# Optimization experiments

Measured on AMD Instinct MI355X. Metric: run time of the kernel, lower is better.

The kernel has to match this reference:

```python
import jax, jax.numpy as jnp
import numpy as np

B, T, IN, HID, LAT = 256, 512, 128, 64, 16

def _mk_lstm(key, in_dim, h_dim, scale):
    k1, k2, k3, k4 = jax.random.split(key, 4)
    return (jax.random.normal(k1, (4 * h_dim, in_dim), jnp.float32) * scale,
            jax.random.normal(k2, (4 * h_dim, h_dim), jnp.float32) * scale,
            jax.random.normal(k3, (4 * h_dim,), jnp.float32) * scale,
            jax.random.normal(k4, (4 * h_dim,), jnp.float32) * scale)

def setup_inputs() -> dict:
    key = jax.random.key(0)
    ks = jax.random.split(key, 5)
    x = jax.random.normal(ks[0], (B, T, IN), jnp.float32)
    out = {"x": x}
    dims = [(IN, HID, "e1"), (HID, LAT, "e2"), (LAT, HID, "d1"), (HID, IN, "d2")]
    for k, (di, dh, nm) in zip(ks[1:], dims):
        scale = 1.0 / np.sqrt(dh)  # pytorch LSTM init range ~ 1/sqrt(hidden)
        Wih, Whh, bih, bhh = _mk_lstm(k, di, dh, scale)
        out[f"Wih_{nm}"], out[f"Whh_{nm}"], out[f"bih_{nm}"], out[f"bhh_{nm}"] = Wih, Whh, bih, bhh
    return out

def lstm(x, Wih, Whh, bih, bhh):
    # x: [B,T,I]; gates ordered i,f,g,o as in torch.nn.LSTM
    H = Whh.shape[1]
    xg = jnp.einsum('bti,gi->btg', x, Wih) + bih + bhh  # [B,T,4H]
    def step(carry, xt):
        h, c = carry
        g = xt + h @ Whh.T
        i, f, gg, o = jnp.split(g, 4, axis=-1)
        c = jax.nn.sigmoid(f) * c + jax.nn.sigmoid(i) * jnp.tanh(gg)
        h = jax.nn.sigmoid(o) * jnp.tanh(c)
        return (h, c), h
    b = x.shape[0]
    h0 = jnp.zeros((b, H), x.dtype)
    _, hs = jax.lax.scan(step, (h0, h0), jnp.swapaxes(xg, 0, 1))
    return jnp.swapaxes(hs, 0, 1)  # [B,T,H]

def reference(x, Wih_e1, Whh_e1, bih_e1, bhh_e1, Wih_e2, Whh_e2, bih_e2, bhh_e2,
              Wih_d1, Whh_d1, bih_d1, bhh_d1, Wih_d2, Whh_d2, bih_d2, bhh_d2):
    # dropout layers are identity at inference
    out = jax.nn.relu(lstm(x, Wih_e1, Whh_e1, bih_e1, bhh_e1))
    out = jax.nn.relu(lstm(out, Wih_e2, Whh_e2, bih_e2, bhh_e2))
    latent = out[:, -1, :]                                  # [B,LAT]
    dec_in = jnp.broadcast_to(latent[:, None, :], (x.shape[0], x.shape[1], latent.shape[-1]))
    out = jax.nn.relu(lstm(dec_in, Wih_d1, Whh_d1, bih_d1, bhh_d1))
    return lstm(out, Wih_d2, Whh_d2, bih_d2, bhh_d2)        # [B,T,IN]
```

## Files before the change

kernel.cpp:

```cpp
#include <hip/hip_runtime.h>


#define BB 256
#define TT 512

typedef _Float16 half2v __attribute__((ext_vector_type(2)));

static __device__ __forceinline__ float dot2(half2v a, half2v b, float c){
  return __builtin_amdgcn_fdot2(a,b,c,false);
}
template<int CTRL>
static __device__ __forceinline__ float qb(float v){
  return __int_as_float(__builtin_amdgcn_update_dpp(0, __float_as_int(v), CTRL, 0xF, 0xF, true));
}
static __device__ __forceinline__ float qsum1(float v){ return v + qb<0xB1>(v); }
static __device__ __forceinline__ float qsum2(float v){ return v + qb<0x4E>(v); }
static __device__ __forceinline__ float hsum8(float v){
  v = qsum1(v); v = qsum2(v); return v + qb<0x141>(v);
}
static __device__ __forceinline__ unsigned packh2(float lo, float hi){
  half2v p; p.x=(_Float16)lo; p.y=(_Float16)hi;
  return __builtin_bit_cast(unsigned, p);
}
static __device__ __forceinline__ half2v ash2(unsigned u){ return __builtin_bit_cast(half2v,u); }
static __device__ __forceinline__ half2v mkh2(float lo, float hi){
  half2v p; p.x=(_Float16)lo; p.y=(_Float16)hi; return p;
}

static __device__ __forceinline__ float lstm_update(int q, float a0, float a1,
                                                    float a2, float a3, float& c){
  float mine = a0;
  mine = (q==1) ? a1 : mine;
  mine = (q==2) ? a2 : mine;
  mine = (q==3) ? a3 : mine;
  const bool isg = (q==2);
  const float arg = isg ? (mine+mine) : mine;
  const float s   = 1.0f/(1.0f + __expf(-arg));
  const float act = isg ? (s+s-1.0f) : s;
  const float bi = qb<0x00>(act);
  const float bf = qb<0x55>(act);
  const float bg = qb<0xAA>(act);
  const float bo = qb<0xFF>(act);
  c = bf*c + bi*bg;
  const float s2 = 1.0f/(1.0f + __expf(-(c+c)));
  return bo*(s2+s2-1.0f);
}

__global__ void __launch_bounds__(512, 2) k_fused(
    const float* __restrict__ x,
    const float* __restrict__ WihE1, const float* __restrict__ WhhE1,
    const float* __restrict__ bihE1, const float* __restrict__ bhhE1,
    const float* __restrict__ WihE2, const float* __restrict__ WhhE2,
    const float* __restrict__ bihE2, const float* __restrict__ bhhE2,
    const float* __restrict__ WihD1, const float* __restrict__ WhhD1,
    const float* __restrict__ bihD1, const float* __restrict__ bhhD1,
    const float* __restrict__ WihD2, const float* __restrict__ WhhD2,
    const float* __restrict__ bihD2, const float* __restrict__ bhhD2,
    float* __restrict__ out)
{
  const int b = blockIdx.x, tid = threadIdx.x;

  __shared__ unsigned wD1L[8*1024];
  __shared__ unsigned vhE [2*96];
  __shared__ unsigned e2op[2*48];
  __shared__ unsigned dop [2*96];
  __shared__ unsigned vhD1[2*32];
  __shared__ float4   bD2L[128];
  __shared__ float4   pD1L[64];
  __shared__ float    latF[16];

  {
    const int o = tid & 7, j = tid >> 3;
    half2v w1[4][12];
    float bias1[4];
#pragma unroll
    for (int g=0; g<4; ++g){
      const int row = g*64 + j;
      bias1[g] = (o==0) ? (bihE1[row]+bhhE1[row]) : 0.0f;
#pragma unroll
      for (int m=0;m<12;++m){
        const int k0 = 24*o + 2*m;
        const float lo = (k0   < 128)? WihE1[row*128+k0]   : WhhE1[row*64 + (k0-128)];
        const float hi = (k0+1 < 128)? WihE1[row*128+k0+1] : WhhE1[row*64 + (k0+1-128)];
        w1[g][m] = mkh2(lo,hi);
      }
    }
    const bool e2act = (tid >= 64 && tid < 128);
    const int q2 = tid & 3, j2 = (tid - 64) >> 2;
    half2v w2[4][12];
    float bias2[4] = {0.f,0.f,0.f,0.f};
    if (e2act){
#pragma unroll
      for (int g=0; g<4; ++g){
        const int row = g*16 + j2;
        bias2[g] = (q2==0) ? (bihE2[row]+bhhE2[row]) : 0.0f;
#pragma unroll
        for (int m=0;m<12;++m){
          const int k0 = 24*q2 + 2*m;
          float lo = 0.0f, hi = 0.0f;
          if (k0 < 64)        lo = WihE2[row*64+k0];
          else if (k0 < 80)   lo = WhhE2[row*16 + (k0-64)];
          if (k0+1 < 64)      hi = WihE2[row*64+k0+1];
          else if (k0+1 < 80) hi = WhhE2[row*16 + (k0+1-64)];
          w2[g][m] = mkh2(lo,hi);
        }
      }
    }
    const bool xact = (tid < 64);
    const float* xrow = x + (size_t)b * (TT*128);
    float2 xa, xb;
    if (xact){
      float2 v0 = *(const float2*)(xrow + 2*tid);
      vhE[tid] = packh2(v0.x, v0.y);
      xa = *(const float2*)(xrow + 128 + 2*tid);
      xb = *(const float2*)(xrow + 256 + 2*tid);
    }
    if (tid >= 128 && tid < 160) vhE[64 + (tid-128)] = 0u;
    if (tid >= 160 && tid < 256) e2op[tid-160] = 0u;
    float c1 = 0.0f, c2 = 0.0f;
    __syncthreads();

#define XSTAGE(T, NXT) do{ if (xact){                                          \
      vhE[(NXT)*96 + tid] = packh2(xa.x, xa.y);                                \
      xa = xb;                                                                 \
      const int t3_ = ((T)+3 < TT) ? ((T)+3) : (TT-1);                         \
      xb = *(const float2*)(xrow + (size_t)t3_*128 + 2*tid);                   \
    } }while(0)

#define E1STEP(T, CUR) do{                                                     \
      float a0=bias1[0], a1=bias1[1], a2=bias1[2], a3=bias1[3];                \
      const uint4* vp = (const uint4*)(vhE + (CUR)*96 + o*12);                 \
      _Pragma("unroll")                                                        \
      for (int r=0;r<3;++r){                                                   \
        const uint4 u = vp[r];                                                 \
        const half2v o0=ash2(u.x), o1=ash2(u.y), o2=ash2(u.z), o3=ash2(u.w);   \
        a0=dot2(w1[0][4*r+0],o0,a0); a1=dot2(w1[1][4*r+0],o0,a1);              \
        a2=dot2(w1[2][4*r+0],o0,a2); a3=dot2(w1[3][4*r+0],o0,a3);              \
        a0=dot2(w1[0][4*r+1],o1,a0); a1=dot2(w1[1][4*r+1],o1,a1);              \
        a2=dot2(w1[2][4*r+1],o1,a2); a3=dot2(w1[3][4*r+1],o1,a3);              \
        a0=dot2(w1[0][4*r+2],o2,a0); a1=dot2(w1[1][4*r+2],o2,a1);              \
        a2=dot2(w1[2][4*r+2],o2,a2); a3=dot2(w1[3][4*r+2],o2,a3);              \
        a0=dot2(w1[0][4*r+3],o3,a0); a1=dot2(w1[1][4*r+3],o3,a1);              \
        a2=dot2(w1[2][4*r+3],o3,a2); a3=dot2(w1[3][4*r+3],o3,a3);              \
      }                                                                        \
      a0=hsum8(a0); a1=hsum8(a1); a2=hsum8(a2); a3=hsum8(a3);                  \
      const float h = lstm_update(o & 3, a0, a1, a2, a3, c1);                  \
      if (o == 0){                                                             \
        ((_Float16*)(vhE + ((CUR)^1)*96))[128 + j] = (_Float16)h;              \
        ((_Float16*)(e2op + (CUR)*48))[j]          = (_Float16)fmaxf(h, 0.0f); \
      }                                                                        \
    }while(0)

#define E2STEP(T2, CP) do{ if (e2act){                                         \
      float a0=bias2[0], a1=bias2[1], a2=bias2[2], a3=bias2[3];                \
      const uint4* vp = (const uint4*)(e2op + (CP)*48 + q2*12);                \
      _Pragma("unroll")                                                        \
      for (int r=0;r<3;++r){                                                   \
        const uint4 u = vp[r];                                                 \
        const half2v o0=ash2(u.x), o1=ash2(u.y), o2=ash2(u.z), o3=ash2(u.w);   \
        a0=dot2(w2[0][4*r+0],o0,a0); a1=dot2(w2[1][4*r+0],o0,a1);              \
        a2=dot2(w2[2][4*r+0],o0,a2); a3=dot2(w2[3][4*r+0],o0,a3);              \
        a0=dot2(w2[0][4*r+1],o1,a0); a1=dot2(w2[1][4*r+1],o1,a1);              \
        a2=dot2(w2[2][4*r+1],o1,a2); a3=dot2(w2[3][4*r+1],o1,a3);              \
        a0=dot2(w2[0][4*r+2],o2,a0); a1=dot2(w2[1][4*r+2],o2,a1);              \
        a2=dot2(w2[2][4*r+2],o2,a2); a3=dot2(w2[3][4*r+2],o2,a3);              \
        a0=dot2(w2[0][4*r+3],o3,a0); a1=dot2(w2[1][4*r+3],o3,a1);              \
        a2=dot2(w2[2][4*r+3],o3,a2); a3=dot2(w2[3][4*r+3],o3,a3);              \
      }                                                                        \
      a0=qsum2(qsum1(a0)); a1=qsum2(qsum1(a1));                                \
      a2=qsum2(qsum1(a2)); a3=qsum2(qsum1(a3));                                \
      const float h = lstm_update(q2, a0, a1, a2, a3, c2);                     \
      if (q2 == 0){                                                            \
        ((_Float16*)(e2op + ((CP)^1)*48))[64 + j2] = (_Float16)h;              \
        if ((T2) == TT-1) latF[j2] = fmaxf(h, 0.0f);                           \
      }                                                                        \
    } }while(0)

    XSTAGE(0, 1); E1STEP(0, 0);
    __syncthreads();
    for (int t = 1; t <= TT-3; t += 2){
      XSTAGE(t, 0);   E1STEP(t, 1);   E2STEP(t-1, 0);
      __syncthreads();
      XSTAGE(t+1, 1); E1STEP(t+1, 0); E2STEP(t, 1);
      __syncthreads();
    }
    XSTAGE(TT-1, 0); E1STEP(TT-1, 1); E2STEP(TT-2, 0);
    __syncthreads();
    E2STEP(TT-1, 1);
    __syncthreads();
#undef XSTAGE
#undef E1STEP
#undef E2STEP
  }
  __syncthreads();
  asm volatile("" ::: "memory");

  {
#pragma unroll
    for (int i=0;i<16;++i){
      const int idx = i*512 + tid;
      const int r = idx >> 10, rem = idx & 1023, l = rem >> 2, d = rem & 3;
      const int jd_ = l >> 2, qd_ = l & 3, g = r >> 1, m = ((r & 1) << 2) + d;
      const int row = g*64 + jd_, k0 = qd_*16 + 2*m;
      wD1L[idx] = packh2(WhhD1[row*64+k0], WhhD1[row*64+k0+1]);
    }
    if (tid < 128){
      float4 bb;
      bb.x = bihD2[0*128+tid] + bhhD2[0*128+tid];
      bb.y = bihD2[1*128+tid] + bhhD2[1*128+tid];
      bb.z = bihD2[2*128+tid] + bhhD2[2*128+tid];
      bb.w = bihD2[3*128+tid] + bhhD2[3*128+tid];
      bD2L[tid] = bb;
    }
    if (tid < 64){
      float4 pp;
#pragma unroll
      for (int g=0; g<4; ++g){
        const int row = g*64 + tid;
        float a = bihD1[row] + bhhD1[row];
#pragma unroll
        for (int i=0;i<16;++i) a = fmaf(WihD1[row*16+i], latF[i], a);
        (&pp.x)[g] = a;
      }
      pD1L[tid] = pp;
    }

    const int qd = tid & 3, jd = tid >> 2;
    half2v wD2[4][24];
#pragma unroll
    for (int g=0; g<4; ++g){
      const int row = g*128 + jd;
#pragma unroll
      for (int m=0;m<24;++m){
        const int k0 = 48*qd + 2*m;
        const float lo = (k0   < 64)? WihD2[row*64+k0]   : WhhD2[row*128+(k0-64)];
        const float hi = (k0+1 < 64)? WihD2[row*64+k0+1] : WhhD2[row*128+(k0+1-64)];
        wD2[g][m] = mkh2(lo,hi);
      }
    }
    const bool d1act = (tid < 256);
    if (tid < 64)                dop[32 + tid] = 0u;
    if (tid >= 64 && tid < 96)   vhD1[tid-64] = 0u;
    float cd1 = 0.0f, cd2 = 0.0f;
    float* orow = out + (size_t)b * (TT*128);
    __syncthreads();

#define D2STEP(T2, C2P) do{                                                    \
      float a0=0.f, a1=0.f, a2=0.f, a3=0.f;                                    \
      const uint4* vp = (const uint4*)(dop + (C2P)*96 + qd*24);                \
      _Pragma("unroll")                                                        \
      for (int r=0;r<6;++r){                                                   \
        const uint4 u = vp[r];                                                 \
        const half2v o0=ash2(u.x),o1=ash2(u.y),o2=ash2(u.z),o3=ash2(u.w);      \
        a0=dot2(wD2[0][4*r+0],o0,a0); a1=dot2(wD2[1][4*r+0],o0,a1);            \
        a2=dot2(wD2[2][4*r+0],o0,a2); a3=dot2(wD2[3][4*r+0],o0,a3);            \
        a0=dot2(wD2[0][4*r+1],o1,a0); a1=dot2(wD2[1][4*r+1],o1,a1);            \
        a2=dot2(wD2[2][4*r+1],o1,a2); a3=dot2(wD2[3][4*r+1],o1,a3);            \
        a0=dot2(wD2[0][4*r+2],o2,a0); a1=dot2(wD2[1][4*r+2],o2,a1);            \
        a2=dot2(wD2[2][4*r+2],o2,a2); a3=dot2(wD2[3][4*r+2],o2,a3);            \
        a0=dot2(wD2[0][4*r+3],o3,a0); a1=dot2(wD2[1][4*r+3],o3,a1);            \
        a2=dot2(wD2[2][4*r+3],o3,a2); a3=dot2(wD2[3][4*r+3],o3,a3);            \
      }                                                                        \
      a0=qsum2(qsum1(a0)); a1=qsum2(qsum1(a1));                                \
      a2=qsum2(qsum1(a2)); a3=qsum2(qsum1(a3));                                \
      const float4 bb = bD2L[jd];                                              \
      a0 += bb.x; a1 += bb.y; a2 += bb.z; a3 += bb.w;                          \
      const float h = lstm_update(qd, a0, a1, a2, a3, cd2);                    \
      if (qd==0){                                                              \
        ((_Float16*)(dop + ((C2P)^1)*96))[64 + jd] = (_Float16)h;              \
        orow[(size_t)(T2)*128 + jd] = h;                                       \
      }                                                                        \
    }while(0)

#define D1STEP(T, CUR) do{ if (d1act){                                         \
      const uint4* ov = (const uint4*)(vhD1 + (CUR)*32 + qd*8);                \
      const uint4 o01 = ov[0], o23 = ov[1];                                    \
      float a0=0.f, a1=0.f, a2=0.f, a3=0.f;                                    \
      {                                                                        \
        const uint4 wA = *(const uint4*)(wD1L + 0*1024 + tid*4);               \
        const uint4 wB = *(const uint4*)(wD1L + 1*1024 + tid*4);               \
        a0=dot2(ash2(wA.x),ash2(o01.x),a0); a0=dot2(ash2(wA.y),ash2(o01.y),a0);\
        a0=dot2(ash2(wA.z),ash2(o01.z),a0); a0=dot2(ash2(wA.w),ash2(o01.w),a0);\
        a0=dot2(ash2(wB.x),ash2(o23.x),a0); a0=dot2(ash2(wB.y),ash2(o23.y),a0);\
        a0=dot2(ash2(wB.z),ash2(o23.z),a0); a0=dot2(ash2(wB.w),ash2(o23.w),a0);\
      }                                                                        \
      {                                                                        \
        const uint4 wA = *(const uint4*)(wD1L + 2*1024 + tid*4);               \
        const uint4 wB = *(const uint4*)(wD1L + 3*1024 + tid*4);               \
        a1=dot2(ash2(wA.x),ash2(o01.x),a1); a1=dot2(ash2(wA.y),ash2(o01.y),a1);\
        a1=dot2(ash2(wA.z),ash2(o01.z),a1); a1=dot2(ash2(wA.w),ash2(o01.w),a1);\
        a1=dot2(ash2(wB.x),ash2(o23.x),a1); a1=dot2(ash2(wB.y),ash2(o23.y),a1);\
        a1=dot2(ash2(wB.z),ash2(o23.z),a1); a1=dot2(ash2(wB.w),ash2(o23.w),a1);\
      }                                                                        \
      {                                                                        \
        const uint4 wA = *(const uint4*)(wD1L + 4*1024 + tid*4);               \
        const uint4 wB = *(const uint4*)(wD1L + 5*1024 + tid*4);               \
        a2=dot2(ash2(wA.x),ash2(o01.x),a2); a2=dot2(ash2(wA.y),ash2(o01.y),a2);\
        a2=dot2(ash2(wA.z),ash2(o01.z),a2); a2=dot2(ash2(wA.w),ash2(o01.w),a2);\
        a2=dot2(ash2(wB.x),ash2(o23.x),a2); a2=dot2(ash2(wB.y),ash2(o23.y),a2);\
        a2=dot2(ash2(wB.z),ash2(o23.z),a2); a2=dot2(ash2(wB.w),ash2(o23.w),a2);\
      }                                                                        \
      {                                                                        \
        const uint4 wA = *(const uint4*)(wD1L + 6*1024 + tid*4);               \
        const uint4 wB = *(const uint4*)(wD1L + 7*1024 + tid*4);               \
        a3=dot2(ash2(wA.x),ash2(o01.x),a3); a3=dot2(ash2(wA.y),ash2(o01.y),a3);\
        a3=dot2(ash2(wA.z),ash2(o01.z),a3); a3=dot2(ash2(wA.w),ash2(o01.w),a3);\
        a3=dot2(ash2(wB.x),ash2(o23.x),a3); a3=dot2(ash2(wB.y),ash2(o23.y),a3);\
        a3=dot2(ash2(wB.z),ash2(o23.z),a3); a3=dot2(ash2(wB.w),ash2(o23.w),a3);\
      }                                                                        \
      a0=qsum2(qsum1(a0)); a1=qsum2(qsum1(a1));                                \
      a2=qsum2(qsum1(a2)); a3=qsum2(qsum1(a3));                                \
      const float4 pj = pD1L[jd];                                              \
      a0 += pj.x; a1 += pj.y; a2 += pj.z; a3 += pj.w;                          \
      const float h = lstm_update(qd, a0, a1, a2, a3, cd1);                    \
      if (qd==0){                                                              \
        ((_Float16*)(vhD1 + ((CUR)^1)*32))[jd] = (_Float16)h;                  \
        ((_Float16*)(dop + (CUR)*96))[jd]      = (_Float16)fmaxf(h,0.0f);      \
      }                                                                        \
    } }while(0)

    D1STEP(0, 0);
    __syncthreads();
    for (int t = 1; t <= TT-3; t += 2){
      D2STEP(t-1, 0); D1STEP(t, 1);
      __syncthreads();
      D2STEP(t, 1);   D1STEP(t+1, 0);
      __syncthreads();
    }
    D2STEP(TT-2, 0); D1STEP(TT-1, 1);
    __syncthreads();
    D2STEP(TT-1, 1);
#undef D2STEP
#undef D1STEP
  }
}

extern "C" void kernel_launch(void* const* d_in, const int* in_sizes, int n_in,
                              void* d_out, int out_size, void* d_ws, size_t ws_size,
                              hipStream_t stream) {
  const float* x      = (const float*)d_in[0];
  const float* WihE1  = (const float*)d_in[1];
  const float* WhhE1  = (const float*)d_in[2];
  const float* bihE1  = (const float*)d_in[3];
  const float* bhhE1  = (const float*)d_in[4];
  const float* WihE2  = (const float*)d_in[5];
  const float* WhhE2  = (const float*)d_in[6];
  const float* bihE2  = (const float*)d_in[7];
  const float* bhhE2  = (const float*)d_in[8];
  const float* WihD1  = (const float*)d_in[9];
  const float* WhhD1  = (const float*)d_in[10];
  const float* bihD1  = (const float*)d_in[11];
  const float* bhhD1  = (const float*)d_in[12];
  const float* WihD2  = (const float*)d_in[13];
  const float* WhhD2  = (const float*)d_in[14];
  const float* bihD2  = (const float*)d_in[15];
  const float* bhhD2  = (const float*)d_in[16];
  float* out = (float*)d_out;

  k_fused<<<BB, 512, 0, stream>>>(x,
      WihE1, WhhE1, bihE1, bhhE1,
      WihE2, WhhE2, bihE2, bhhE2,
      WihD1, WhhD1, bihD1, bhhD1,
      WihD2, WhhD2, bihD2, bhhD2,
      out);
}
```

Before: 871.9 us.

## Hold D1 recurrent weights in registers across all 512 threads and spread x staging

Decoder layer 1's recurrent weights now live in registers rather than a 32 KB shared-memory table. The work is spread over all 512 threads, each with 8 lanes per hidden unit and an 8-lane DPP reduction, replacing 256 threads that read weights from LDS on every step. The x-staging loads are also spread across one 8-lane group in each wave instead of the first 64 threads. The aim is to cut per-step LDS traffic and free shared memory, at the cost of extra VGPRs and an extra reduction stage on the critical recurrent path.

After: 984.8 us. 13.0% more time.

```diff
diff --git a/kernel.cpp b/kernel.cpp
--- a/kernel.cpp
+++ b/kernel.cpp
@@ -60,7 +60,6 @@
 {
   const int b = blockIdx.x, tid = threadIdx.x;
 
-  __shared__ unsigned wD1L[8*1024];
   __shared__ unsigned vhE [2*96];
   __shared__ unsigned e2op[2*48];
   __shared__ unsigned dop [2*96];
@@ -106,14 +105,15 @@
         }
       }
     }
-    const bool xact = (tid < 64);
+    const bool xact = ((tid & 63) < 8);
+    const int  xl   = ((tid >> 6) << 3) | (tid & 7);
     const float* xrow = x + (size_t)b * (TT*128);
     float2 xa, xb;
     if (xact){
-      float2 v0 = *(const float2*)(xrow + 2*tid);
-      vhE[tid] = packh2(v0.x, v0.y);
-      xa = *(const float2*)(xrow + 128 + 2*tid);
-      xb = *(const float2*)(xrow + 256 + 2*tid);
+      float2 v0 = *(const float2*)(xrow + 2*xl);
+      vhE[xl] = packh2(v0.x, v0.y);
+      xa = *(const float2*)(xrow + 128 + 2*xl);
+      xb = *(const float2*)(xrow + 256 + 2*xl);
     }
     if (tid >= 128 && tid < 160) vhE[64 + (tid-128)] = 0u;
     if (tid >= 160 && tid < 256) e2op[tid-160] = 0u;
@@ -121,10 +121,10 @@
     __syncthreads();
 
 #define XSTAGE(T, NXT) do{ if (xact){                                          \
-      vhE[(NXT)*96 + tid] = packh2(xa.x, xa.y);                                \
+      vhE[(NXT)*96 + xl] = packh2(xa.x, xa.y);                                 \
       xa = xb;                                                                 \
       const int t3_ = ((T)+3 < TT) ? ((T)+3) : (TT-1);                         \
-      xb = *(const float2*)(xrow + (size_t)t3_*128 + 2*tid);                   \
+      xb = *(const float2*)(xrow + (size_t)t3_*128 + 2*xl);                    \
     } }while(0)
 
 #define E1STEP(T, CUR) do{                                                     \
@@ -196,14 +196,6 @@
   asm volatile("" ::: "memory");
 
   {
-#pragma unroll
-    for (int i=0;i<16;++i){
-      const int idx = i*512 + tid;
-      const int r = idx >> 10, rem = idx & 1023, l = rem >> 2, d = rem & 3;
-      const int jd_ = l >> 2, qd_ = l & 3, g = r >> 1, m = ((r & 1) << 2) + d;
-      const int row = g*64 + jd_, k0 = qd_*16 + 2*m;
-      wD1L[idx] = packh2(WhhD1[row*64+k0], WhhD1[row*64+k0+1]);
-    }
     if (tid < 128){
       float4 bb;
       bb.x = bihD2[0*128+tid] + bhhD2[0*128+tid];
@@ -238,7 +230,17 @@
         wD2[g][m] = mkh2(lo,hi);
       }
     }
-    const bool d1act = (tid < 256);
+    const int o8 = tid & 7, j1d = tid >> 3;
+    half2v wd1[4][4];
+#pragma unroll
+    for (int g=0; g<4; ++g){
+      const int row = g*64 + j1d;
+#pragma unroll
+      for (int m=0;m<4;++m){
+        const int k0 = o8*8 + 2*m;
+        wd1[g][m] = mkh2(WhhD1[row*64+k0], WhhD1[row*64+k0+1]);
+      }
+    }
     if (tid < 64)                dop[32 + tid] = 0u;
     if (tid >= 64 && tid < 96)   vhD1[tid-64] = 0u;
     float cd1 = 0.0f, cd2 = 0.0f;
@@ -272,52 +274,27 @@
       }                                                                        \
     }while(0)
 
-#define D1STEP(T, CUR) do{ if (d1act){                                         \
-      const uint4* ov = (const uint4*)(vhD1 + (CUR)*32 + qd*8);                \
-      const uint4 o01 = ov[0], o23 = ov[1];                                    \
+#define D1STEP(T, CUR) do{                                                     \
+      const uint4 u = *(const uint4*)(vhD1 + (CUR)*32 + o8*4);                 \
+      const half2v o0=ash2(u.x),o1=ash2(u.y),o2=ash2(u.z),o3=ash2(u.w);        \
       float a0=0.f, a1=0.f, a2=0.f, a3=0.f;                                    \
-      {                                                                        \
-        const uint4 wA = *(const uint4*)(wD1L + 0*1024 + tid*4);               \
-        const uint4 wB = *(const uint4*)(wD1L + 1*1024 + tid*4);               \
-        a0=dot2(ash2(wA.x),ash2(o01.x),a0); a0=dot2(ash2(wA.y),ash2(o01.y),a0);\
-        a0=dot2(ash2(wA.z),ash2(o01.z),a0); a0=dot2(ash2(wA.w),ash2(o01.w),a0);\
-        a0=dot2(ash2(wB.x),ash2(o23.x),a0); a0=dot2(ash2(wB.y),ash2(o23.y),a0);\
-        a0=dot2(ash2(wB.z),ash2(o23.z),a0); a0=dot2(ash2(wB.w),ash2(o23.w),a0);\
-      }                                                                        \
-      {                                                                        \
-        const uint4 wA = *(const uint4*)(wD1L + 2*1024 + tid*4);               \
-        const uint4 wB = *(const uint4*)(wD1L + 3*1024 + tid*4);               \
-        a1=dot2(ash2(wA.x),ash2(o01.x),a1); a1=dot2(ash2(wA.y),ash2(o01.y),a1);\
-        a1=dot2(ash2(wA.z),ash2(o01.z),a1); a1=dot2(ash2(wA.w),ash2(o01.w),a1);\
-        a1=dot2(ash2(wB.x),ash2(o23.x),a1); a1=dot2(ash2(wB.y),ash2(o23.y),a1);\
-        a1=dot2(ash2(wB.z),ash2(o23.z),a1); a1=dot2(ash2(wB.w),ash2(o23.w),a1);\
-      }                                                                        \
-      {                                                                        \
-        const uint4 wA = *(const uint4*)(wD1L + 4*1024 + tid*4);               \
-        const uint4 wB = *(const uint4*)(wD1L + 5*1024 + tid*4);               \
-        a2=dot2(ash2(wA.x),ash2(o01.x),a2); a2=dot2(ash2(wA.y),ash2(o01.y),a2);\
-        a2=dot2(ash2(wA.z),ash2(o01.z),a2); a2=dot2(ash2(wA.w),ash2(o01.w),a2);\
-        a2=dot2(ash2(wB.x),ash2(o23.x),a2); a2=dot2(ash2(wB.y),ash2(o23.y),a2);\
-        a2=dot2(ash2(wB.z),ash2(o23.z),a2); a2=dot2(ash2(wB.w),ash2(o23.w),a2);\
-      }                                                                        \
-      {                                                                        \
-        const uint4 wA = *(const uint4*)(wD1L + 6*1024 + tid*4);               \
-        const uint4 wB = *(const uint4*)(wD1L + 7*1024 + tid*4);               \
-        a3=dot2(ash2(wA.x),ash2(o01.x),a3); a3=dot2(ash2(wA.y),ash2(o01.y),a3);\
-        a3=dot2(ash2(wA.z),ash2(o01.z),a3); a3=dot2(ash2(wA.w),ash2(o01.w),a3);\
-        a3=dot2(ash2(wB.x),ash2(o23.x),a3); a3=dot2(ash2(wB.y),ash2(o23.y),a3);\
-        a3=dot2(ash2(wB.z),ash2(o23.z),a3); a3=dot2(ash2(wB.w),ash2(o23.w),a3);\
-      }                                                                        \
-      a0=qsum2(qsum1(a0)); a1=qsum2(qsum1(a1));                                \
-      a2=qsum2(qsum1(a2)); a3=qsum2(qsum1(a3));                                \
-      const float4 pj = pD1L[jd];                                              \
+      a0=dot2(wd1[0][0],o0,a0); a1=dot2(wd1[1][0],o0,a1);                      \
+      a2=dot2(wd1[2][0],o0,a2); a3=dot2(wd1[3][0],o0,a3);                      \
+      a0=dot2(wd1[0][1],o1,a0); a1=dot2(wd1[1][1],o1,a1);                      \
+      a2=dot2(wd1[2][1],o1,a2); a3=dot2(wd1[3][1],o1,a3);                      \
+      a0=dot2(wd1[0][2],o2,a0); a1=dot2(wd1[1][2],o2,a1);                      \
+      a2=dot2(wd1[2][2],o2,a2); a3=dot2(wd1[3][2],o2,a3);                      \
+      a0=dot2(wd1[0][3],o3,a0); a1=dot2(wd1[1][3],o3,a1);                      \
+      a2=dot2(wd1[2][3],o3,a2); a3=dot2(wd1[3][3],o3,a3);                      \
+      a0=hsum8(a0); a1=hsum8(a1); a2=hsum8(a2); a3=hsum8(a3);                  \
+      const float4 pj = pD1L[j1d];                                             \
       a0 += pj.x; a1 += pj.y; a2 += pj.z; a3 += pj.w;                          \
-      const float h = lstm_update(qd, a0, a1, a2, a3, cd1);                    \
-      if (qd==0){                                                              \
-        ((_Float16*)(vhD1 + ((CUR)^1)*32))[jd] = (_Float16)h;                  \
-        ((_Float16*)(dop + (CUR)*96))[jd]      = (_Float16)fmaxf(h,0.0f);      \
-      }                                                                        \
-    } }while(0)
+      const float h = lstm_update(tid & 3, a0, a1, a2, a3, cd1);               \
+      if (o8==0){                                                              \
+        ((_Float16*)(vhD1 + ((CUR)^1)*32))[j1d] = (_Float16)h;                 \
+        ((_Float16*)(dop + (CUR)*96))[j1d]      = (_Float16)fmaxf(h,0.0f);     \
+      }                                                                        \
+    }while(0)
 
     D1STEP(0, 0);
     __syncthreads();
```
